# Kernel optimization log

Measured on AMD Instinct MI355X. Metric: run time of the kernel, lower is better.

Reference implementation:

```python
import math
import jax, jax.numpy as jnp
import numpy as np

DIM = 1024
NUM_HEADS = 16
HEAD_DIM = DIM // NUM_HEADS
SCALE = HEAD_DIM ** -0.5
ROPE_BASE = 10000.0


def _rope(x):
    # x: [b, h, t, d]; rotate-half RoPE as in the torch module
    b, h, t, d = x.shape
    half = d // 2
    freqs = jnp.exp(-math.log(ROPE_BASE) * jnp.arange(half, dtype=jnp.float32) / half)
    pos = jnp.arange(t, dtype=jnp.float32)
    angles = pos[:, None] * freqs[None, :]          # [t, half]
    sin = jnp.sin(angles)[None, None, :, :]
    cos = jnp.cos(angles)[None, None, :, :]
    x1, x2 = x[..., :half], x[..., half:]
    return jnp.concatenate([x1 * cos - x2 * sin, x1 * sin + x2 * cos], axis=-1)


def setup_inputs() -> dict:
    key = jax.random.key(0)
    k1, k2, k3, k4 = jax.random.split(key, 4)
    b, t = 2, 2048
    x = jax.random.normal(k1, (b, t, DIM), dtype=jnp.float32)
    # nn.Linear(dim, 3*dim, bias=False): store as [in, out] for x @ W
    w_qkv = jax.random.normal(k2, (DIM, 3 * DIM), dtype=jnp.float32) * (DIM ** -0.5)
    w_proj = jax.random.normal(k3, (DIM, DIM), dtype=jnp.float32) * (DIM ** -0.5)
    b_proj = jax.random.normal(k4, (DIM,), dtype=jnp.float32) * 0.02
    return {"x": x, "w_qkv": w_qkv, "w_proj": w_proj, "b_proj": b_proj}


def reference(x, w_qkv, w_proj, b_proj):
    b, t, c = x.shape
    h, hd = NUM_HEADS, HEAD_DIM
    qkv = (x @ w_qkv).reshape(b, t, 3, h, hd)
    qkv = jnp.transpose(qkv, (2, 0, 3, 1, 4))      # [3, b, h, t, hd]
    q, k, v = qkv[0], qkv[1], qkv[2]
    q, k = _rope(q), _rope(k)
    attn = jnp.einsum('bhqd,bhkd->bhqk', q, k) * SCALE
    causal_mask = jnp.triu(jnp.ones((t, t), dtype=bool), k=1)
    attn = jnp.where(causal_mask[None, None], -jnp.inf, attn)
    attn = jax.nn.softmax(attn, axis=-1)
    out = jnp.einsum('bhqk,bhkd->bhqd', attn, v)
    out = jnp.transpose(out, (0, 2, 1, 3)).reshape(b, t, c)
    return out @ w_proj + b_proj
```

## Files before the change

kernel.cpp:

```cpp
#include <hip/hip_runtime.h>
#include <math.h>

typedef unsigned short u16;
typedef unsigned int u32;
typedef __bf16 bfrag8 __attribute__((ext_vector_type(8)));
typedef float f32x4 __attribute__((ext_vector_type(4)));

#define B_ 2
#define T_ 2048
#define H_ 16
#define D_ 64
#define C_ 1024
#define NQKV_ 3072

#define MFMA_BF16(a, b, c) __builtin_amdgcn_mfma_f32_16x16x32_bf16((a), (b), (c), 0, 0, 0)

__device__ __forceinline__ u16 f2bf(float f) {
  u32 u = __builtin_bit_cast(u32, f);
  u += 0x7fffu + ((u >> 16) & 1u);
  return (u16)(u >> 16);
}

__device__ __forceinline__ void load_lds16(const u16* gp, u16* lp) {
  __builtin_amdgcn_global_load_lds(
      (const __attribute__((address_space(1))) u32*)(const void*)gp,
      (__attribute__((address_space(3))) u32*)(void*)lp, 16, 0, 0);
}

__global__ __launch_bounds__(256) void convert_x(const float* __restrict__ src,
                                                 u16* __restrict__ dst) {
  size_t i = ((size_t)blockIdx.x * 256 + threadIdx.x) * 8;
  const float* s = src + i;
  float4 a = *(const float4*)s, b = *(const float4*)(s + 4);
  union { uint4 v; u16 h[8]; } t;
  t.h[0] = f2bf(a.x); t.h[1] = f2bf(a.y); t.h[2] = f2bf(a.z); t.h[3] = f2bf(a.w);
  t.h[4] = f2bf(b.x); t.h[5] = f2bf(b.y); t.h[6] = f2bf(b.z); t.h[7] = f2bf(b.w);
  *(uint4*)(dst + i) = t.v;
}

__global__ __launch_bounds__(256) void transpose_w(const float* __restrict__ src,
                                                   u16* __restrict__ dst, int K, int N) {
  __shared__ u16 tile[64][65];
  int bx = blockIdx.x * 64;
  int by = blockIdx.y * 64;
  for (int idx = threadIdx.x; idx < 4096; idx += 256) {
    int r = idx >> 6, c = idx & 63;
    tile[r][c] = f2bf(src[(size_t)(by + r) * N + bx + c]);
  }
  __syncthreads();
  for (int idx = threadIdx.x; idx < 4096; idx += 256) {
    int r = idx >> 6, c = idx & 63;
    dst[(size_t)(bx + r) * K + by + c] = tile[c][r];
  }
}

__global__ __launch_bounds__(256) void gemm_qkv_rope(const u16* __restrict__ X,
                                                     const u16* __restrict__ WT,
                                                     u16* __restrict__ qb,
                                                     u16* __restrict__ kb,
                                                     u16* __restrict__ vb) {
  const int K = C_;
  __shared__ __align__(16) u16 As[128 * 32];
  __shared__ __align__(16) u16 Bs[128 * 32];
  int tid = threadIdx.x;
  int lane = tid & 63, wave = tid >> 6;
  int quad = lane >> 4, lr = lane & 15;
  int m0 = blockIdx.y * 128, n0 = blockIdx.x * 128;
  int wrow = (wave >> 1) * 64, wcol = (wave & 1) * 64;
  int r0 = wave * 32;
  int srow = lane >> 2, skc = (lane & 3) * 8;

  f32x4 zero = {0.f, 0.f, 0.f, 0.f};
  f32x4 acc[4][4];
#pragma unroll
  for (int i = 0; i < 4; i++)
#pragma unroll
    for (int j = 0; j < 4; j++) acc[i][j] = zero;

  const u16* ga0 = X + (size_t)(m0 + r0 + srow) * K + skc;
  const u16* ga1 = X + (size_t)(m0 + r0 + 16 + srow) * K + skc;
  const u16* gb0 = WT + (size_t)(n0 + r0 + srow) * K + skc;
  const u16* gb1 = WT + (size_t)(n0 + r0 + 16 + srow) * K + skc;

  for (int k0 = 0; k0 < K; k0 += 32) {
    load_lds16(ga0 + k0, &As[r0 * 32]);
    load_lds16(ga1 + k0, &As[(r0 + 16) * 32]);
    load_lds16(gb0 + k0, &Bs[r0 * 32]);
    load_lds16(gb1 + k0, &Bs[(r0 + 16) * 32]);
    __syncthreads();
    bfrag8 af[4], bfr[4];
#pragma unroll
    for (int i = 0; i < 4; i++)
      af[i] = *(const bfrag8*)&As[(wrow + i * 16 + lr) * 32 + quad * 8];
#pragma unroll
    for (int j = 0; j < 4; j++)
      bfr[j] = *(const bfrag8*)&Bs[(wcol + j * 16 + lr) * 32 + quad * 8];
#pragma unroll
    for (int i = 0; i < 4; i++)
#pragma unroll
      for (int j = 0; j < 4; j++) acc[i][j] = MFMA_BF16(af[i], bfr[j], acc[i][j]);
    __syncthreads();
  }

  int colbase = n0 + wcol;
  int which = colbase >> 10;
  int h = (colbase & 1023) >> 6;
  u16* dst = which == 0 ? qb : (which == 1 ? kb : vb);
  float sc0 = (which == 0) ? 0.125f : 1.0f;
  float fr0 = __expf(-0.28782313662425574f * (float)lr);
  float fr1 = __expf(-0.28782313662425574f * (float)(16 + lr));
#pragma unroll
  for (int i = 0; i < 4; i++) {
#pragma unroll
    for (int r = 0; r < 4; r++) {
      int m = m0 + wrow + i * 16 + quad * 4 + r;
      int b = m >> 11, tt = m & 2047;
      size_t base = ((size_t)(b * H_ + h) * T_ + tt) * D_;
      if (which < 2) {
        float sn, cs;
        __sincosf((float)tt * fr0, &sn, &cs);
        dst[base + lr] = f2bf((acc[i][0][r] * cs - acc[i][2][r] * sn) * sc0);
        dst[base + lr + 32] = f2bf((acc[i][0][r] * sn + acc[i][2][r] * cs) * sc0);
        __sincosf((float)tt * fr1, &sn, &cs);
        dst[base + 16 + lr] = f2bf((acc[i][1][r] * cs - acc[i][3][r] * sn) * sc0);
        dst[base + 48 + lr] = f2bf((acc[i][1][r] * sn + acc[i][3][r] * cs) * sc0);
      } else {
#pragma unroll
        for (int j = 0; j < 4; j++) dst[base + j * 16 + lr] = f2bf(acc[i][j][r]);
      }
    }
  }
}

__global__ __launch_bounds__(256) void transpose_v(const u16* __restrict__ v,
                                                   u16* __restrict__ vt) {
  __shared__ u16 tile[64][72];
  int t0 = blockIdx.x * 64;
  int bh = blockIdx.y;
  const u16* src = v + (size_t)bh * T_ * D_;
  u16* dst = vt + (size_t)bh * D_ * T_;
  for (int idx = threadIdx.x; idx < 512; idx += 256) {
    int r = idx >> 3, c8 = (idx & 7) * 8;
    *(uint4*)&tile[r][c8] = *(const uint4*)(src + (size_t)(t0 + r) * D_ + c8);
  }
  __syncthreads();
  for (int idx = threadIdx.x; idx < 512; idx += 256) {
    int d = idx >> 3, t8 = (idx & 7) * 8;
    union { uint4 u; u16 s[8]; } p;
#pragma unroll
    for (int e = 0; e < 8; e++) p.s[e] = tile[t8 + e][d];
    *(uint4*)(dst + (size_t)d * T_ + t0 + t8) = p.u;
  }
}

__global__ __launch_bounds__(256) void attn_k(const u16* __restrict__ qb,
                                              const u16* __restrict__ kb,
                                              const u16* __restrict__ vtb,
                                              u16* __restrict__ ob) {
  __shared__ __align__(16) u16 Ks[2][64 * 64];
  __shared__ __align__(16) u16 Vt[2][64 * 64];
  __shared__ __align__(16) u16 Pst[4][16 * 72];
  int tid = threadIdx.x;
  int lane = tid & 63, wave = tid >> 6;
  int quad = lane >> 4, lr = lane & 15;
  int i = blockIdx.x;
  int bq = 31 - (i >> 5);
  int bh = i & 31;
  int b = bh >> 4, h = bh & 15;
  const u16* Q = qb + (size_t)bh * T_ * D_;
  const u16* Kp = kb + (size_t)bh * T_ * D_;
  const u16* Vp = vtb + (size_t)bh * D_ * T_;
  int qr0 = bq * 64 + wave * 16;
  int r0 = wave * 16;
  int sr = lane >> 3, sc = (lane & 7) * 8;

  bfrag8 qf[2];
#pragma unroll
  for (int ks = 0; ks < 2; ks++)
    qf[ks] = *(const bfrag8*)(Q + (size_t)(qr0 + lr) * D_ + ks * 32 + quad * 8);

  f32x4 zero = {0.f, 0.f, 0.f, 0.f};
  f32x4 o[4];
#pragma unroll
  for (int nn = 0; nn < 4; nn++) o[nn] = zero;
  float psum = 0.f;

  const u16* gk = Kp + (size_t)(r0 + sr) * D_ + sc;
  const u16* gv = Vp + (size_t)(r0 + sr) * T_ + sc;
  int niter = bq + 1;

  load_lds16(gk, &Ks[0][r0 * 64]);
  load_lds16(gk + (size_t)8 * D_, &Ks[0][(r0 + 8) * 64]);
  load_lds16(gv, &Vt[0][r0 * 64]);
  load_lds16(gv + (size_t)8 * T_, &Vt[0][(r0 + 8) * 64]);

  int buf = 0;
  int qloc = wave * 16 + lr;
  for (int it = 0; it < niter; it++) {
    __syncthreads();
    if (it + 1 < niter) {
      int tkn = (it + 1) * 64;
      load_lds16(gk + (size_t)tkn * D_, &Ks[buf ^ 1][r0 * 64]);
      load_lds16(gk + (size_t)(tkn + 8) * D_, &Ks[buf ^ 1][(r0 + 8) * 64]);
      load_lds16(gv + tkn, &Vt[buf ^ 1][r0 * 64]);
      load_lds16(gv + (size_t)8 * T_ + tkn, &Vt[buf ^ 1][(r0 + 8) * 64]);
    }
    const u16* ks_ = Ks[buf];
    const u16* vt_ = Vt[buf];

    f32x4 s[4];
#pragma unroll
    for (int j = 0; j < 4; j++) s[j] = zero;
#pragma unroll
    for (int ks = 0; ks < 2; ks++)
#pragma unroll
      for (int j = 0; j < 4; j++) {
        bfrag8 kf = *(const bfrag8*)&ks_[(j * 16 + lr) * 64 + ks * 32 + quad * 8];
        s[j] = MFMA_BF16(kf, qf[ks], s[j]);
      }

    bool edge = (it == bq);
#pragma unroll
    for (int j = 0; j < 4; j++) {
      float p[4];
#pragma unroll
      for (int r = 0; r < 4; r++) {
        float e = __expf(s[j][r]);
        if (edge) {
          int kvloc = j * 16 + quad * 4 + r;
          e = (kvloc <= qloc) ? e : 0.f;
        }
        p[r] = e;
        psum += e;
      }
      u32 u0 = __builtin_bit_cast(u32, p[0]) + 0x8000u;
      u32 u1 = __builtin_bit_cast(u32, p[1]) + 0x8000u;
      u32 u2 = __builtin_bit_cast(u32, p[2]) + 0x8000u;
      u32 u3 = __builtin_bit_cast(u32, p[3]) + 0x8000u;
      uint2 pk;
      pk.x = (u0 >> 16) | (u1 & 0xffff0000u);
      pk.y = (u2 >> 16) | (u3 & 0xffff0000u);
      *(uint2*)&Pst[wave][lr * 72 + j * 16 + quad * 4] = pk;
    }

#pragma unroll
    for (int ks = 0; ks < 2; ks++) {
      bfrag8 pf = *(const bfrag8*)&Pst[wave][lr * 72 + ks * 32 + quad * 8];
#pragma unroll
      for (int nn = 0; nn < 4; nn++) {
        bfrag8 vf = *(const bfrag8*)&vt_[(nn * 16 + lr) * 64 + ks * 32 + quad * 8];
        o[nn] = MFMA_BF16(pf, vf, o[nn]);
      }
    }
    buf ^= 1;
  }

  float l = psum;
  l += __shfl_xor(l, 16, 64);
  l += __shfl_xor(l, 32, 64);
  float linv = 1.0f / l;

#pragma unroll
  for (int r = 0; r < 4; r++) {
    float lrec = __shfl(linv, quad * 4 + r, 64);
    int row = qr0 + quad * 4 + r;
#pragma unroll
    for (int nn = 0; nn < 4; nn++)
      ob[(size_t)(b * T_ + row) * C_ + h * 64 + nn * 16 + lr] = f2bf(o[nn][r] * lrec);
  }
}

__global__ __launch_bounds__(256) void gemm_proj(const u16* __restrict__ A,
                                                 const u16* __restrict__ WT,
                                                 const float* __restrict__ bias,
                                                 float* __restrict__ out) {
  const int K = C_;
  __shared__ __align__(16) u16 As[128 * 32];
  __shared__ __align__(16) u16 Bs[128 * 32];
  int tid = threadIdx.x;
  int lane = tid & 63, wave = tid >> 6;
  int quad = lane >> 4, lr = lane & 15;
  int m0 = blockIdx.y * 128, n0 = blockIdx.x * 128;
  int wrow = (wave >> 1) * 64, wcol = (wave & 1) * 64;
  int r0 = wave * 32;
  int srow = lane >> 2, skc = (lane & 3) * 8;

  f32x4 zero = {0.f, 0.f, 0.f, 0.f};
  f32x4 acc[4][4];
#pragma unroll
  for (int i = 0; i < 4; i++)
#pragma unroll
    for (int j = 0; j < 4; j++) acc[i][j] = zero;

  const u16* ga0 = A + (size_t)(m0 + r0 + srow) * K + skc;
  const u16* ga1 = A + (size_t)(m0 + r0 + 16 + srow) * K + skc;
  const u16* gb0 = WT + (size_t)(n0 + r0 + srow) * K + skc;
  const u16* gb1 = WT + (size_t)(n0 + r0 + 16 + srow) * K + skc;

  for (int k0 = 0; k0 < K; k0 += 32) {
    load_lds16(ga0 + k0, &As[r0 * 32]);
    load_lds16(ga1 + k0, &As[(r0 + 16) * 32]);
    load_lds16(gb0 + k0, &Bs[r0 * 32]);
    load_lds16(gb1 + k0, &Bs[(r0 + 16) * 32]);
    __syncthreads();
    bfrag8 af[4], bfr[4];
#pragma unroll
    for (int i = 0; i < 4; i++)
      af[i] = *(const bfrag8*)&As[(wrow + i * 16 + lr) * 32 + quad * 8];
#pragma unroll
    for (int j = 0; j < 4; j++)
      bfr[j] = *(const bfrag8*)&Bs[(wcol + j * 16 + lr) * 32 + quad * 8];
#pragma unroll
    for (int i = 0; i < 4; i++)
#pragma unroll
      for (int j = 0; j < 4; j++) acc[i][j] = MFMA_BF16(af[i], bfr[j], acc[i][j]);
    __syncthreads();
  }

#pragma unroll
  for (int i = 0; i < 4; i++)
#pragma unroll
    for (int r = 0; r < 4; r++) {
      int m = m0 + wrow + i * 16 + quad * 4 + r;
#pragma unroll
      for (int j = 0; j < 4; j++) {
        int n = n0 + wcol + j * 16 + lr;
        out[(size_t)m * C_ + n] = acc[i][j][r] + bias[n];
      }
    }
}

extern "C" void kernel_launch(void* const* d_in, const int* in_sizes, int n_in,
                              void* d_out, int out_size, void* d_ws, size_t ws_size,
                              hipStream_t stream) {
  const float* x = (const float*)d_in[0];
  const float* w_qkv = (const float*)d_in[1];
  const float* w_proj = (const float*)d_in[2];
  const float* b_proj = (const float*)d_in[3];

  char* w = (char*)d_ws;
  u16* xb = (u16*)(w + 256);
  u16* vtb = xb;
  u16* regA = xb + (size_t)4096 * 1024;
  u16* wqkvT = regA;
  u16* abuf = regA;
  u16* wprojT = regA + (size_t)4096 * 1024;
  u16* qbuf = wprojT + (size_t)1024 * 1024;
  u16* kbuf = qbuf + (size_t)B_ * H_ * T_ * D_;
  u16* vbuf = kbuf + (size_t)B_ * H_ * T_ * D_;

  convert_x<<<2048, 256, 0, stream>>>(x, xb);
  transpose_w<<<dim3(NQKV_ / 64, C_ / 64), 256, 0, stream>>>(w_qkv, wqkvT, C_, NQKV_);
  transpose_w<<<dim3(C_ / 64, C_ / 64), 256, 0, stream>>>(w_proj, wprojT, C_, C_);
  gemm_qkv_rope<<<dim3(NQKV_ / 128, (B_ * T_) / 128), 256, 0, stream>>>(xb, wqkvT, qbuf, kbuf, vbuf);
  transpose_v<<<dim3(T_ / 64, B_ * H_), 256, 0, stream>>>(vbuf, vtb);
  attn_k<<<1024, 256, 0, stream>>>(qbuf, kbuf, vtb, abuf);
  gemm_proj<<<dim3(C_ / 128, (B_ * T_) / 128), 256, 0, stream>>>(abuf, wprojT, b_proj, (float*)d_out);
}
```

Before: 215.5 us.

## Double-buffer LDS tiles in both GEMMs and shrink proj tile to 64 rows

Both the QKV and projection GEMMs now keep two LDS stages, issuing the global-to-LDS loads for the next K slice before computing on the current one. This removes one barrier per iteration and overlaps memory latency with MFMA work. The projection GEMM also moves from 128x128 to 64x128 tiles with each wave owning 64x32, doubling its block count (256 to 512) so more CUs are busy. The cost is double the shared memory per block and less reuse per loaded tile in the projection. Safety with a single barrier depends on the async LDS loads completing before the barrier, which relies on the compiler's waitcnt handling.

```diff
diff --git a/kernel.cpp b/kernel.cpp
--- a/kernel.cpp
+++ b/kernel.cpp
@@ -60,8 +60,8 @@
                                                      u16* __restrict__ kb,
                                                      u16* __restrict__ vb) {
   const int K = C_;
-  __shared__ __align__(16) u16 As[128 * 32];
-  __shared__ __align__(16) u16 Bs[128 * 32];
+  __shared__ __align__(16) u16 As[2][128 * 32];
+  __shared__ __align__(16) u16 Bs[2][128 * 32];
   int tid = threadIdx.x;
   int lane = tid & 63, wave = tid >> 6;
   int quad = lane >> 4, lr = lane & 15;
@@ -82,24 +82,32 @@
   const u16* gb0 = WT + (size_t)(n0 + r0 + srow) * K + skc;
   const u16* gb1 = WT + (size_t)(n0 + r0 + 16 + srow) * K + skc;
 
+  load_lds16(ga0, &As[0][r0 * 32]);
+  load_lds16(ga1, &As[0][(r0 + 16) * 32]);
+  load_lds16(gb0, &Bs[0][r0 * 32]);
+  load_lds16(gb1, &Bs[0][(r0 + 16) * 32]);
+
+  int buf = 0;
   for (int k0 = 0; k0 < K; k0 += 32) {
-    load_lds16(ga0 + k0, &As[r0 * 32]);
-    load_lds16(ga1 + k0, &As[(r0 + 16) * 32]);
-    load_lds16(gb0 + k0, &Bs[r0 * 32]);
-    load_lds16(gb1 + k0, &Bs[(r0 + 16) * 32]);
     __syncthreads();
+    if (k0 + 32 < K) {
+      load_lds16(ga0 + k0 + 32, &As[buf ^ 1][r0 * 32]);
+      load_lds16(ga1 + k0 + 32, &As[buf ^ 1][(r0 + 16) * 32]);
+      load_lds16(gb0 + k0 + 32, &Bs[buf ^ 1][r0 * 32]);
+      load_lds16(gb1 + k0 + 32, &Bs[buf ^ 1][(r0 + 16) * 32]);
+    }
     bfrag8 af[4], bfr[4];
 #pragma unroll
     for (int i = 0; i < 4; i++)
-      af[i] = *(const bfrag8*)&As[(wrow + i * 16 + lr) * 32 + quad * 8];
+      af[i] = *(const bfrag8*)&As[buf][(wrow + i * 16 + lr) * 32 + quad * 8];
 #pragma unroll
     for (int j = 0; j < 4; j++)
-      bfr[j] = *(const bfrag8*)&Bs[(wcol + j * 16 + lr) * 32 + quad * 8];
+      bfr[j] = *(const bfrag8*)&Bs[buf][(wcol + j * 16 + lr) * 32 + quad * 8];
 #pragma unroll
     for (int i = 0; i < 4; i++)
 #pragma unroll
       for (int j = 0; j < 4; j++) acc[i][j] = MFMA_BF16(af[i], bfr[j], acc[i][j]);
-    __syncthreads();
+    buf ^= 1;
   }
 
   int colbase = n0 + wcol;
@@ -275,55 +283,59 @@
                                                  const float* __restrict__ bias,
                                                  float* __restrict__ out) {
   const int K = C_;
-  __shared__ __align__(16) u16 As[128 * 32];
-  __shared__ __align__(16) u16 Bs[128 * 32];
+  __shared__ __align__(16) u16 As[2][64 * 32];
+  __shared__ __align__(16) u16 Bs[2][128 * 32];
   int tid = threadIdx.x;
   int lane = tid & 63, wave = tid >> 6;
   int quad = lane >> 4, lr = lane & 15;
-  int m0 = blockIdx.y * 128, n0 = blockIdx.x * 128;
-  int wrow = (wave >> 1) * 64, wcol = (wave & 1) * 64;
-  int r0 = wave * 32;
+  int m0 = blockIdx.y * 64, n0 = blockIdx.x * 128;
+  int wcol = wave * 32;
   int srow = lane >> 2, skc = (lane & 3) * 8;
 
   f32x4 zero = {0.f, 0.f, 0.f, 0.f};
-  f32x4 acc[4][4];
+  f32x4 acc[4][2];
 #pragma unroll
   for (int i = 0; i < 4; i++)
 #pragma unroll
-    for (int j = 0; j < 4; j++) acc[i][j] = zero;
-
-  const u16* ga0 = A + (size_t)(m0 + r0 + srow) * K + skc;
-  const u16* ga1 = A + (size_t)(m0 + r0 + 16 + srow) * K + skc;
-  const u16* gb0 = WT + (size_t)(n0 + r0 + srow) * K + skc;
-  const u16* gb1 = WT + (size_t)(n0 + r0 + 16 + srow) * K + skc;
-
+    for (int j = 0; j < 2; j++) acc[i][j] = zero;
+
+  const u16* ga = A + (size_t)(m0 + wave * 16 + srow) * K + skc;
+  const u16* gb0 = WT + (size_t)(n0 + wave * 32 + srow) * K + skc;
+  const u16* gb1 = WT + (size_t)(n0 + wave * 32 + 16 + srow) * K + skc;
+
+  load_lds16(ga, &As[0][wave * 16 * 32]);
+  load_lds16(gb0, &Bs[0][wave * 32 * 32]);
+  load_lds16(gb1, &Bs[0][(wave * 32 + 16) * 32]);
+
+  int buf = 0;
   for (int k0 = 0; k0 < K; k0 += 32) {
-    load_lds16(ga0 + k0, &As[r0 * 32]);
-    load_lds16(ga1 + k0, &As[(r0 + 16) * 32]);
-    load_lds16(gb0 + k0, &Bs[r0 * 32]);
-    load_lds16(gb1 + k0, &Bs[(r0 + 16) * 32]);
     __syncthreads();
-    bfrag8 af[4], bfr[4];
+    if (k0 + 32 < K) {
+      load_lds16(ga + k0 + 32, &As[buf ^ 1][wave * 16 * 32]);
+      load_lds16(gb0 + k0 + 32, &Bs[buf ^ 1][wave * 32 * 32]);
+      load_lds16(gb1 + k0 + 32, &Bs[buf ^ 1][(wave * 32 + 16) * 32]);
+    }
+    bfrag8 af[4], bfr[2];
 #pragma unroll
     for (int i = 0; i < 4; i++)
-      af[i] = *(const bfrag8*)&As[(wrow + i * 16 + lr) * 32 + quad * 8];
-#pragma unroll
-    for (int j = 0; j < 4; j++)
-      bfr[j] = *(const bfrag8*)&Bs[(wcol + j * 16 + lr) * 32 + quad * 8];
+      af[i] = *(const bfrag8*)&As[buf][(i * 16 + lr) * 32 + quad * 8];
+#pragma unroll
+    for (int j = 0; j < 2; j++)
+      bfr[j] = *(const bfrag8*)&Bs[buf][(wcol + j * 16 + lr) * 32 + quad * 8];
 #pragma unroll
     for (int i = 0; i < 4; i++)
 #pragma unroll
-      for (int j = 0; j < 4; j++) acc[i][j] = MFMA_BF16(af[i], bfr[j], acc[i][j]);
-    __syncthreads();
+      for (int j = 0; j < 2; j++) acc[i][j] = MFMA_BF16(af[i], bfr[j], acc[i][j]);
+    buf ^= 1;
   }
 
 #pragma unroll
   for (int i = 0; i < 4; i++)
 #pragma unroll
     for (int r = 0; r < 4; r++) {
-      int m = m0 + wrow + i * 16 + quad * 4 + r;
-#pragma unroll
-      for (int j = 0; j < 4; j++) {
+      int m = m0 + i * 16 + quad * 4 + r;
+#pragma unroll
+      for (int j = 0; j < 2; j++) {
         int n = n0 + wcol + j * 16 + lr;
         out[(size_t)m * C_ + n] = acc[i][j][r] + bias[n];
       }
@@ -355,5 +367,5 @@
   gemm_qkv_rope<<<dim3(NQKV_ / 128, (B_ * T_) / 128), 256, 0, stream>>>(xb, wqkvT, qbuf, kbuf, vbuf);
   transpose_v<<<dim3(T_ / 64, B_ * H_), 256, 0, stream>>>(vbuf, vtb);
   attn_k<<<1024, 256, 0, stream>>>(qbuf, kbuf, vtb, abuf);
-  gemm_proj<<<dim3(C_ / 128, (B_ * T_) / 128), 256, 0, stream>>>(abuf, wprojT, b_proj, (float*)d_out);
-}
+  gemm_proj<<<dim3(C_ / 128, (B_ * T_) / 64), 256, 0, stream>>>(abuf, wprojT, b_proj, (float*)d_out);
+}
```

Result: faster. 204.2 us (-5.2%).
